# Kernel tuning notes

Hardware: AMD Instinct MI355X
Metric: run time of the kernel (lower is better)

## Reference

```python
import jax, jax.numpy as jnp
import numpy as np

N = 200000
D = 256
B = 512  # fixed num_segments (batch.max()+1 in the torch code)
LN_EPS = 1e-5


def _layernorm(h, gamma, beta):
    mu = jnp.mean(h, axis=-1, keepdims=True)
    var = jnp.var(h, axis=-1, keepdims=True)
    return (h - mu) * jax.lax.rsqrt(var + LN_EPS) * gamma + beta


def setup_inputs() -> dict:
    key = jax.random.key(0)
    ks = jax.random.split(key, 10)
    x = jax.random.normal(ks[0], (N, D), dtype=jnp.float32)
    batch = jnp.sort(jax.random.randint(ks[1], (N,), 0, B)).astype(jnp.int64)
    s = 0.05
    return {
        "x": x,
        "batch": batch,
        "vn_embed": jax.random.normal(ks[2], (1, D), dtype=jnp.float32) * 0.02,
        "W1": jax.random.normal(ks[3], (D, D), dtype=jnp.float32) * s,
        "b1": jnp.zeros((D,), dtype=jnp.float32),
        "g1": jnp.ones((D,), dtype=jnp.float32),
        "be1": jnp.zeros((D,), dtype=jnp.float32),
        "W2": jax.random.normal(ks[4], (D, D), dtype=jnp.float32) * s,
        "b2": jnp.zeros((D,), dtype=jnp.float32),
        "g2": jnp.ones((D,), dtype=jnp.float32),
        "be2": jnp.zeros((D,), dtype=jnp.float32),
        "Wg": jax.random.normal(ks[5], (2 * D, D), dtype=jnp.float32) * s,
        "bg": jnp.zeros((D,), dtype=jnp.float32),
    }


def reference(x, batch, vn_embed, W1, b1, g1, be1, W2, b2, g2, be2, Wg, bg):
    # scatter-mean: per-graph average of node features  [B, D]
    seg_sum = jax.ops.segment_sum(x, batch, num_segments=B)
    cnt = jax.ops.segment_sum(jnp.ones((x.shape[0],), x.dtype), batch, num_segments=B)
    node_agg = seg_sum / jnp.maximum(cnt, 1.0)[:, None]
    # node_to_vn: Linear + GELU(exact) + LayerNorm (dropout = identity at eval)
    vn_update = _layernorm(jax.nn.gelu(node_agg @ W1 + b1, approximate=False), g1, be1)
    vn_state = vn_embed + vn_update  # vn_embed broadcasts [1,D] -> [B,D]
    # gather broadcast back to nodes + vn_to_node MLP
    vn_broadcast = vn_state[batch]  # [N, D]
    node_update = _layernorm(jax.nn.gelu(vn_broadcast @ W2 + b2, approximate=False), g2, be2)
    # sigmoid gate on concat + gated residual
    gate = jax.nn.sigmoid(jnp.concatenate([x, node_update], axis=-1) @ Wg + bg)
    x_out = x + gate * node_update
    return (x_out, vn_state)
```

## Files before the change

### kernel.cpp

```cpp
#include <hip/hip_runtime.h>
#include <hip/hip_bf16.h>
#include <math.h>

#define DIM 256
#define B_SEG 512
#define LN_EPS 1e-5f
#define CHUNK 64

typedef __attribute__((ext_vector_type(8))) short bf16x8;
typedef __attribute__((ext_vector_type(4))) float f32x4;

__device__ __forceinline__ float gelu_exact(float v) {
    return 0.5f * v * (1.0f + erff(v * 0.70710678118654752f));
}

__device__ __forceinline__ unsigned int pack2bf(float a, float b) {
    unsigned int ua = (unsigned int)__bfloat16_as_ushort(__float2bfloat16(a));
    unsigned int ub = (unsigned int)__bfloat16_as_ushort(__float2bfloat16(b));
    return ua | (ub << 16);
}

__device__ __forceinline__ void async16(const void* g, void* l) {
    __builtin_amdgcn_global_load_lds(
        (const __attribute__((address_space(1))) void*)(g),
        (__attribute__((address_space(3))) void*)(l), 16, 0, 0);
}

__global__ __launch_bounds__(256) void k_wprep(const float* __restrict__ Wg,
                                               __hip_bfloat16* __restrict__ Wt2) {
    int k = blockIdx.x;
    int c = threadIdx.x;
    Wt2[((size_t)(k >> 3) << 11) + (c << 3) + (k & 7)] = __float2bfloat16(Wg[(size_t)k * DIM + c]);
}

__global__ __launch_bounds__(256) void k_segsum(const float* __restrict__ x,
                                                const int* __restrict__ batch,
                                                float* __restrict__ sums,
                                                float* __restrict__ cnt,
                                                __hip_bfloat16* __restrict__ xbf,
                                                int n, int emit) {
    const int i0 = blockIdx.x * CHUNK;
    if (i0 >= n) return;
    const int t    = threadIdx.x;
    const int lane = t & 63;
    const int d4   = lane * 4;
    const int rg   = t >> 6;

    int   bt[16];
    float4 v[16];
    #pragma unroll
    for (int j = 0; j < 16; ++j) {
        int i = i0 + rg + 4 * j;
        bt[j] = (i < n) ? batch[i] : -1;
    }
    #pragma unroll
    for (int j = 0; j < 16; ++j) {
        int i = i0 + rg + 4 * j;
        v[j] = (i < n) ? *(const float4*)(x + (size_t)i * DIM + d4)
                       : make_float4(0.f, 0.f, 0.f, 0.f);
    }

    if (emit) {
        #pragma unroll
        for (int j = 0; j < 16; ++j) {
            int i = i0 + rg + 4 * j;
            if (i < n) {
                uint2 pk;
                pk.x = pack2bf(v[j].x, v[j].y);
                pk.y = pack2bf(v[j].z, v[j].w);
                *(uint2*)((char*)xbf + (size_t)i * 512 + ((d4 * 2) ^ ((i & 7) << 4))) = pk;
            }
        }
    }

    float4 acc = make_float4(0.f, 0.f, 0.f, 0.f);
    int cur = -1, run = 0;
    #pragma unroll
    for (int j = 0; j < 16; ++j) {
        if (bt[j] != cur) {
            if (cur >= 0) {
                atomicAdd(&sums[(size_t)cur * DIM + d4 + 0], acc.x);
                atomicAdd(&sums[(size_t)cur * DIM + d4 + 1], acc.y);
                atomicAdd(&sums[(size_t)cur * DIM + d4 + 2], acc.z);
                atomicAdd(&sums[(size_t)cur * DIM + d4 + 3], acc.w);
                if (d4 == 0) atomicAdd(&cnt[cur], (float)run);
            }
            acc = make_float4(0.f, 0.f, 0.f, 0.f);
            run = 0; cur = bt[j];
        }
        acc.x += v[j].x; acc.y += v[j].y; acc.z += v[j].z; acc.w += v[j].w;
        run++;
    }
    if (cur >= 0) {
        atomicAdd(&sums[(size_t)cur * DIM + d4 + 0], acc.x);
        atomicAdd(&sums[(size_t)cur * DIM + d4 + 1], acc.y);
        atomicAdd(&sums[(size_t)cur * DIM + d4 + 2], acc.z);
        atomicAdd(&sums[(size_t)cur * DIM + d4 + 3], acc.w);
        if (d4 == 0) atomicAdd(&cnt[cur], (float)run);
    }
}

__global__ __launch_bounds__(256) void k_vn(const float* __restrict__ sums,
                                            const float* __restrict__ cnt,
                                            const float* __restrict__ vn_embed,
                                            const float* __restrict__ W1, const float* __restrict__ b1,
                                            const float* __restrict__ g1, const float* __restrict__ be1,
                                            const float* __restrict__ W2, const float* __restrict__ b2,
                                            const float* __restrict__ g2, const float* __restrict__ be2,
                                            const float* __restrict__ Wg, const float* __restrict__ bg,
                                            float* __restrict__ vn_state_out,
                                            float* __restrict__ nu,
                                            float* __restrict__ gpart) {
    __shared__ float sIn[DIM];
    __shared__ float sRed[DIM];
    __shared__ float sRed2[DIM];
    const int b = blockIdx.x;
    const int d = threadIdx.x;

    float c = cnt[b];
    float denom = fmaxf(c, 1.0f);
    sIn[d] = sums[(size_t)b * DIM + d] / denom;
    __syncthreads();

    float h0 = 0.f, h1 = 0.f, h2a = 0.f, h3 = 0.f;
    for (int k = 0; k < DIM; k += 4) {
        h0  = fmaf(sIn[k + 0], W1[(size_t)(k + 0) * DIM + d], h0);
        h1  = fmaf(sIn[k + 1], W1[(size_t)(k + 1) * DIM + d], h1);
        h2a = fmaf(sIn[k + 2], W1[(size_t)(k + 2) * DIM + d], h2a);
        h3  = fmaf(sIn[k + 3], W1[(size_t)(k + 3) * DIM + d], h3);
    }
    float h = gelu_exact(b1[d] + ((h0 + h1) + (h2a + h3)));

    sRed[d] = h; sRed2[d] = h * h;
    __syncthreads();
    for (int s = 128; s > 0; s >>= 1) {
        if (d < s) { sRed[d] += sRed[d + s]; sRed2[d] += sRed2[d + s]; }
        __syncthreads();
    }
    float mu = sRed[0] * (1.0f / DIM);
    float var = fmaxf(sRed2[0] * (1.0f / DIM) - mu * mu, 0.0f);
    float rs = rsqrtf(var + LN_EPS);
    float vnst = vn_embed[d] + ((h - mu) * rs * g1[d] + be1[d]);
    vn_state_out[(size_t)b * DIM + d] = vnst;
    __syncthreads();
    sIn[d] = vnst;
    __syncthreads();

    float g0 = 0.f, g1a = 0.f, g2a = 0.f, g3 = 0.f;
    for (int k = 0; k < DIM; k += 4) {
        g0  = fmaf(sIn[k + 0], W2[(size_t)(k + 0) * DIM + d], g0);
        g1a = fmaf(sIn[k + 1], W2[(size_t)(k + 1) * DIM + d], g1a);
        g2a = fmaf(sIn[k + 2], W2[(size_t)(k + 2) * DIM + d], g2a);
        g3  = fmaf(sIn[k + 3], W2[(size_t)(k + 3) * DIM + d], g3);
    }
    float h2 = gelu_exact(b2[d] + ((g0 + g1a) + (g2a + g3)));

    sRed[d] = h2; sRed2[d] = h2 * h2;
    __syncthreads();
    for (int s = 128; s > 0; s >>= 1) {
        if (d < s) { sRed[d] += sRed[d + s]; sRed2[d] += sRed2[d + s]; }
        __syncthreads();
    }
    float mu2 = sRed[0] * (1.0f / DIM);
    float var2 = fmaxf(sRed2[0] * (1.0f / DIM) - mu2 * mu2, 0.0f);
    float rs2 = rsqrtf(var2 + LN_EPS);
    float nud = (h2 - mu2) * rs2 * g2[d] + be2[d];
    nu[(size_t)b * DIM + d] = nud;
    __syncthreads();
    sIn[d] = nud;
    __syncthreads();

    float p0 = 0.f, p1 = 0.f, p2 = 0.f, p3 = 0.f;
    for (int k = 0; k < DIM; k += 4) {
        p0 = fmaf(sIn[k + 0], Wg[(size_t)(DIM + k + 0) * DIM + d], p0);
        p1 = fmaf(sIn[k + 1], Wg[(size_t)(DIM + k + 1) * DIM + d], p1);
        p2 = fmaf(sIn[k + 2], Wg[(size_t)(DIM + k + 2) * DIM + d], p2);
        p3 = fmaf(sIn[k + 3], Wg[(size_t)(DIM + k + 3) * DIM + d], p3);
    }
    gpart[(size_t)b * DIM + d] = bg[d] + ((p0 + p1) + (p2 + p3));
}

__global__ __launch_bounds__(256, 4) void k_gate_bf(const __hip_bfloat16* __restrict__ xbf,
                                                    const int* __restrict__ batch,
                                                    const __hip_bfloat16* __restrict__ Wt2,
                                                    const float* __restrict__ nu,
                                                    const float* __restrict__ gpart,
                                                    float* __restrict__ xout,
                                                    int n) {
    __shared__ __align__(16) char sA[64 * 512];

    const int tid  = threadIdx.x;
    const int wave = tid >> 6;
    const int lane = tid & 63;
    const int r15  = lane & 15;
    const int kq   = lane >> 4;
    const size_t i0 = (size_t)blockIdx.x * 64;

    const char* gsrc = (const char*)xbf + i0 * 512;
    #pragma unroll
    for (int j = 0; j < 8; ++j)
        async16(gsrc + j * 4096 + tid * 16, sA + j * 4096 + wave * 1024);
    __syncthreads();

    f32x4 acc[4][4];
    #pragma unroll
    for (int m = 0; m < 4; ++m)
        #pragma unroll
        for (int nn = 0; nn < 4; ++nn)
            acc[m][nn] = (f32x4){0.f, 0.f, 0.f, 0.f};

    #pragma unroll
    for (int ks = 0; ks < 8; ++ks) {
        bf16x8 a[4], b[4];
        #pragma unroll
        for (int nn = 0; nn < 4; ++nn) {
            int c = wave * 64 + nn * 16 + r15;
            b[nn] = *(const bf16x8*)(Wt2 + ((size_t)(ks * 4 + kq) << 11) + (c << 3));
        }
        #pragma unroll
        for (int m = 0; m < 4; ++m) {
            int r = m * 16 + r15;
            a[m] = *(const bf16x8*)(sA + r * 512 + ((ks * 64 + kq * 16) ^ ((r & 7) << 4)));
        }
        #pragma unroll
        for (int m = 0; m < 4; ++m)
            #pragma unroll
            for (int nn = 0; nn < 4; ++nn)
                acc[m][nn] = __builtin_amdgcn_mfma_f32_16x16x32_bf16(a[m], b[nn], acc[m][nn], 0, 0, 0);
    }

    #pragma unroll
    for (int m = 0; m < 4; ++m) {
        #pragma unroll
        for (int q = 0; q < 4; ++q) {
            int rr = m * 16 + kq * 4 + q;
            long node = (long)(i0 + rr);
            if (node >= n) continue;
            int bb = batch[node];
            #pragma unroll
            for (int nn = 0; nn < 4; ++nn) {
                int col = wave * 64 + nn * 16 + r15;
                float pre = acc[m][nn][q] + gpart[bb * DIM + col];
                float e = __expf(-pre);
                float gte = __builtin_amdgcn_rcpf(1.0f + e);
                float xres = __bfloat162float(
                    *(const __hip_bfloat16*)(sA + rr * 512 + ((2 * col) ^ ((rr & 7) << 4))));
                xout[(size_t)node * DIM + col] = xres + gte * nu[bb * DIM + col];
            }
        }
    }
}

__global__ __launch_bounds__(256) void k_gate_fp(const float* __restrict__ x,
                                                 const int* __restrict__ batch,
                                                 const __hip_bfloat16* __restrict__ Wt2,
                                                 const float* __restrict__ nu,
                                                 const float* __restrict__ gpart,
                                                 float* __restrict__ xout,
                                                 int n) {
    __shared__ __align__(16) char sA[32 * 512];

    const int tid  = threadIdx.x;
    const int wave = tid >> 6;
    const int lane = tid & 63;
    const int r15  = lane & 15;
    const int kq   = lane >> 4;
    const int i0   = blockIdx.x * 32;

    float4 av0[4], av1[4];
    #pragma unroll
    for (int j = 0; j < 4; ++j) {
        int v = j * 256 + tid;
        int r = v >> 5;
        int k8 = v & 31;
        int node = i0 + r;
        if (node < n) {
            const float* p = x + (size_t)node * DIM + k8 * 8;
            av0[j] = *(const float4*)p;
            av1[j] = *(const float4*)(p + 4);
        } else {
            av0[j] = make_float4(0.f, 0.f, 0.f, 0.f);
            av1[j] = av0[j];
        }
    }
    #pragma unroll
    for (int j = 0; j < 4; ++j) {
        int v = j * 256 + tid;
        int r = v >> 5;
        int k8 = v & 31;
        uint4 pk;
        pk.x = pack2bf(av0[j].x, av0[j].y);
        pk.y = pack2bf(av0[j].z, av0[j].w);
        pk.z = pack2bf(av1[j].x, av1[j].y);
        pk.w = pack2bf(av1[j].z, av1[j].w);
        *(uint4*)(sA + r * 512 + ((k8 * 16) ^ ((r & 7) << 4))) = pk;
    }
    __syncthreads();

    f32x4 acc[2][4];
    #pragma unroll
    for (int m = 0; m < 2; ++m)
        #pragma unroll
        for (int nn = 0; nn < 4; ++nn)
            acc[m][nn] = (f32x4){0.f, 0.f, 0.f, 0.f};

    #pragma unroll
    for (int ks = 0; ks < 8; ++ks) {
        bf16x8 a[2], b[4];
        #pragma unroll
        for (int nn = 0; nn < 4; ++nn) {
            int c = wave * 64 + nn * 16 + r15;
            b[nn] = *(const bf16x8*)(Wt2 + ((size_t)(ks * 4 + kq) << 11) + (c << 3));
        }
        #pragma unroll
        for (int m = 0; m < 2; ++m) {
            int r = m * 16 + r15;
            a[m] = *(const bf16x8*)(sA + r * 512 + ((ks * 64 + kq * 16) ^ ((r & 7) << 4)));
        }
        #pragma unroll
        for (int m = 0; m < 2; ++m)
            #pragma unroll
            for (int nn = 0; nn < 4; ++nn)
                acc[m][nn] = __builtin_amdgcn_mfma_f32_16x16x32_bf16(a[m], b[nn], acc[m][nn], 0, 0, 0);
    }

    #pragma unroll
    for (int m = 0; m < 2; ++m) {
        #pragma unroll
        for (int q = 0; q < 4; ++q) {
            int rr = m * 16 + kq * 4 + q;
            int node = i0 + rr;
            if (node >= n) continue;
            int bb = batch[node];
            #pragma unroll
            for (int nn = 0; nn < 4; ++nn) {
                int col = wave * 64 + nn * 16 + r15;
                float pre = acc[m][nn][q] + gpart[bb * DIM + col];
                float e = __expf(-pre);
                float gte = __builtin_amdgcn_rcpf(1.0f + e);
                float xres = __bfloat162float(
                    *(const __hip_bfloat16*)(sA + rr * 512 + ((2 * col) ^ ((rr & 7) << 4))));
                xout[(size_t)node * DIM + col] = xres + gte * nu[bb * DIM + col];
            }
        }
    }
}

extern "C" void kernel_launch(void* const* d_in, const int* in_sizes, int n_in,
                              void* d_out, int out_size, void* d_ws, size_t ws_size,
                              hipStream_t stream) {
    const float* x        = (const float*)d_in[0];
    const int*   batch    = (const int*)d_in[1];
    const float* vn_embed = (const float*)d_in[2];
    const float* W1  = (const float*)d_in[3];
    const float* b1  = (const float*)d_in[4];
    const float* g1  = (const float*)d_in[5];
    const float* be1 = (const float*)d_in[6];
    const float* W2  = (const float*)d_in[7];
    const float* b2  = (const float*)d_in[8];
    const float* g2  = (const float*)d_in[9];
    const float* be2 = (const float*)d_in[10];
    const float* Wg  = (const float*)d_in[11];
    const float* bg  = (const float*)d_in[12];

    const int n = in_sizes[0] / DIM;

    float* out = (float*)d_out;
    float* xout = out;
    float* vn_state_out = out + (size_t)n * DIM;

    float* ws    = (float*)d_ws;
    float* sums  = ws;
    float* cnt   = sums + (size_t)B_SEG * DIM;
    float* nu    = cnt + B_SEG;
    float* gpart = nu + (size_t)B_SEG * DIM;
    __hip_bfloat16* Wt2 = (__hip_bfloat16*)(gpart + (size_t)B_SEG * DIM);
    __hip_bfloat16* xbf = Wt2 + (size_t)DIM * DIM;

    const size_t base_bytes = ((size_t)B_SEG * DIM * 3 + B_SEG) * 4 + (size_t)DIM * DIM * 2;
    const int nt64 = (n + 63) / 64;
    const size_t need = base_bytes + (size_t)nt64 * 64 * 512;
    const bool use_bf = (ws_size >= need);

    hipMemsetAsync(d_ws, 0, ((size_t)B_SEG * DIM + B_SEG) * sizeof(float), stream);

    k_wprep<<<DIM, DIM, 0, stream>>>(Wg, Wt2);

    int nblk1 = (n + CHUNK - 1) / CHUNK;
    k_segsum<<<nblk1, 256, 0, stream>>>(x, batch, sums, cnt, xbf, n, use_bf ? 1 : 0);

    k_vn<<<B_SEG, 256, 0, stream>>>(sums, cnt, vn_embed,
                                    W1, b1, g1, be1,
                                    W2, b2, g2, be2,
                                    Wg, bg,
                                    vn_state_out, nu, gpart);

    if (use_bf) {
        k_gate_bf<<<nt64, 256, 0, stream>>>(xbf, batch, Wt2, nu, gpart, xout, n);
    } else {
        int nblk3 = (n + 31) / 32;
        k_gate_fp<<<nblk3, 256, 0, stream>>>(x, batch, Wt2, nu, gpart, xout, n);
    }
}
```

Measured before the change: 220.1 us.

## Split bf16 conversion from segment sum and sum from bf16 copy

Moves the fp32-to-bf16 conversion of x into its own grid-stride kernel. The segment-sum kernel then reads the bf16 copy with 16-byte loads instead of fp32. A separate fp32 segment-sum kernel covers the fallback path. The aim is to lighten the segsum kernel's registers and load width, at the cost of an extra kernel launch, an extra pass over the bf16 buffer, and segment means computed from bf16-rounded inputs.

```diff
diff --git a/kernel.cpp b/kernel.cpp
--- a/kernel.cpp
+++ b/kernel.cpp
@@ -5,7 +5,6 @@
 #define DIM 256
 #define B_SEG 512
 #define LN_EPS 1e-5f
-#define CHUNK 64
 
 typedef __attribute__((ext_vector_type(8))) short bf16x8;
 typedef __attribute__((ext_vector_type(4))) float f32x4;
@@ -18,6 +17,10 @@
     unsigned int ua = (unsigned int)__bfloat16_as_ushort(__float2bfloat16(a));
     unsigned int ub = (unsigned int)__bfloat16_as_ushort(__float2bfloat16(b));
     return ua | (ub << 16);
+}
+
+__device__ __forceinline__ float bf2f(short s) {
+    return __uint_as_float(((unsigned int)(unsigned short)s) << 16);
 }
 
 __device__ __forceinline__ void async16(const void* g, void* l) {
@@ -33,70 +36,94 @@
     Wt2[((size_t)(k >> 3) << 11) + (c << 3) + (k & 7)] = __float2bfloat16(Wg[(size_t)k * DIM + c]);
 }
 
-__global__ __launch_bounds__(256) void k_segsum(const float* __restrict__ x,
+__global__ __launch_bounds__(256) void k_convert(const float* __restrict__ x,
+                                                 __hip_bfloat16* __restrict__ xbf,
+                                                 int n) {
+    const int t    = threadIdx.x;
+    const int lane = t & 63;
+    const int rg   = t >> 6;
+    const int step = gridDim.x * 64;
+    for (int base = blockIdx.x * 64; base < n; base += step) {
+        const int r0 = base + rg * 16;
+        float4 v[16];
+        #pragma unroll
+        for (int j = 0; j < 16; ++j) {
+            int r = r0 + j;
+            v[j] = (r < n) ? *(const float4*)(x + (size_t)r * DIM + lane * 4)
+                           : make_float4(0.f, 0.f, 0.f, 0.f);
+        }
+        __builtin_amdgcn_sched_barrier(0);
+        #pragma unroll
+        for (int j = 0; j < 16; ++j) {
+            int r = r0 + j;
+            if (r < n) {
+                uint2 pk;
+                pk.x = pack2bf(v[j].x, v[j].y);
+                pk.y = pack2bf(v[j].z, v[j].w);
+                *(uint2*)((char*)xbf + (size_t)r * 512 + ((lane * 8) ^ ((r & 7) << 4))) = pk;
+            }
+        }
+    }
+}
+
+__global__ __launch_bounds__(256) void k_segsum(const __hip_bfloat16* __restrict__ xbf,
                                                 const int* __restrict__ batch,
                                                 float* __restrict__ sums,
                                                 float* __restrict__ cnt,
-                                                __hip_bfloat16* __restrict__ xbf,
-                                                int n, int emit) {
-    const int i0 = blockIdx.x * CHUNK;
+                                                int n) {
+    const int i0 = blockIdx.x * 64;
     if (i0 >= n) return;
     const int t    = threadIdx.x;
     const int lane = t & 63;
-    const int d4   = lane * 4;
     const int rg   = t >> 6;
-
-    int   bt[16];
-    float4 v[16];
-    #pragma unroll
-    for (int j = 0; j < 16; ++j) {
-        int i = i0 + rg + 4 * j;
-        bt[j] = (i < n) ? batch[i] : -1;
-    }
-    #pragma unroll
-    for (int j = 0; j < 16; ++j) {
-        int i = i0 + rg + 4 * j;
-        v[j] = (i < n) ? *(const float4*)(x + (size_t)i * DIM + d4)
-                       : make_float4(0.f, 0.f, 0.f, 0.f);
-    }
-
-    if (emit) {
-        #pragma unroll
-        for (int j = 0; j < 16; ++j) {
-            int i = i0 + rg + 4 * j;
-            if (i < n) {
-                uint2 pk;
-                pk.x = pack2bf(v[j].x, v[j].y);
-                pk.y = pack2bf(v[j].z, v[j].w);
-                *(uint2*)((char*)xbf + (size_t)i * 512 + ((d4 * 2) ^ ((i & 7) << 4))) = pk;
-            }
-        }
-    }
-
-    float4 acc = make_float4(0.f, 0.f, 0.f, 0.f);
+    const int half = lane >> 5;
+    const int li   = lane & 31;
+    const int d8   = li * 8;
+    const int R0   = i0 + rg * 16;
+
+    int    bt[8];
+    bf16x8 w[8];
+    #pragma unroll
+    for (int j = 0; j < 8; ++j) {
+        int r = R0 + half + 2 * j;
+        bt[j] = (r < n) ? batch[r] : -1;
+    }
+    #pragma unroll
+    for (int j = 0; j < 8; ++j) {
+        int r = R0 + half + 2 * j;
+        if (r < n) {
+            w[j] = *(const bf16x8*)((const char*)xbf + (size_t)r * 512 +
+                                    ((d8 * 2) ^ ((r & 7) << 4)));
+        } else {
+            w[j] = (bf16x8){0, 0, 0, 0, 0, 0, 0, 0};
+        }
+    }
+    __builtin_amdgcn_sched_barrier(0);
+
+    float acc[8] = {0.f, 0.f, 0.f, 0.f, 0.f, 0.f, 0.f, 0.f};
     int cur = -1, run = 0;
     #pragma unroll
-    for (int j = 0; j < 16; ++j) {
+    for (int j = 0; j < 8; ++j) {
         if (bt[j] != cur) {
             if (cur >= 0) {
-                atomicAdd(&sums[(size_t)cur * DIM + d4 + 0], acc.x);
-                atomicAdd(&sums[(size_t)cur * DIM + d4 + 1], acc.y);
-                atomicAdd(&sums[(size_t)cur * DIM + d4 + 2], acc.z);
-                atomicAdd(&sums[(size_t)cur * DIM + d4 + 3], acc.w);
-                if (d4 == 0) atomicAdd(&cnt[cur], (float)run);
+                #pragma unroll
+                for (int e = 0; e < 8; ++e)
+                    atomicAdd(&sums[(size_t)cur * DIM + d8 + e], acc[e]);
+                if (li == 0) atomicAdd(&cnt[cur], (float)run);
             }
-            acc = make_float4(0.f, 0.f, 0.f, 0.f);
+            #pragma unroll
+            for (int e = 0; e < 8; ++e) acc[e] = 0.f;
             run = 0; cur = bt[j];
         }
-        acc.x += v[j].x; acc.y += v[j].y; acc.z += v[j].z; acc.w += v[j].w;
+        #pragma unroll
+        for (int e = 0; e < 8; ++e) acc[e] += bf2f(w[j][e]);
         run++;
     }
     if (cur >= 0) {
-        atomicAdd(&sums[(size_t)cur * DIM + d4 + 0], acc.x);
-        atomicAdd(&sums[(size_t)cur * DIM + d4 + 1], acc.y);
-        atomicAdd(&sums[(size_t)cur * DIM + d4 + 2], acc.z);
-        atomicAdd(&sums[(size_t)cur * DIM + d4 + 3], acc.w);
-        if (d4 == 0) atomicAdd(&cnt[cur], (float)run);
+        #pragma unroll
+        for (int e = 0; e < 8; ++e)
+            atomicAdd(&sums[(size_t)cur * DIM + d8 + e], acc[e]);
+        if (li == 0) atomicAdd(&cnt[cur], (float)run);
     }
 }
 
@@ -251,6 +278,47 @@
     }
 }
 
+__global__ __launch_bounds__(256) void k_segsum_fp(const float* __restrict__ x,
+                                                   const int* __restrict__ batch,
+                                                   float* __restrict__ sums,
+                                                   float* __restrict__ cnt,
+                                                   int n) {
+    const int i0 = blockIdx.x * 64;
+    if (i0 >= n) return;
+    const int t    = threadIdx.x;
+    const int lane = t & 63;
+    const int d4   = lane * 4;
+    const int rg   = t >> 6;
+    float4 acc = make_float4(0.f, 0.f, 0.f, 0.f);
+    int cur = -1, run = 0;
+    for (int j = 0; j < 16; ++j) {
+        int i = i0 + rg + 4 * j;
+        if (i >= n) break;
+        int b = batch[i];
+        if (b != cur) {
+            if (cur >= 0) {
+                atomicAdd(&sums[(size_t)cur * DIM + d4 + 0], acc.x);
+                atomicAdd(&sums[(size_t)cur * DIM + d4 + 1], acc.y);
+                atomicAdd(&sums[(size_t)cur * DIM + d4 + 2], acc.z);
+                atomicAdd(&sums[(size_t)cur * DIM + d4 + 3], acc.w);
+                if (d4 == 0) atomicAdd(&cnt[cur], (float)run);
+            }
+            acc = make_float4(0.f, 0.f, 0.f, 0.f);
+            run = 0; cur = b;
+        }
+        float4 v = *(const float4*)(x + (size_t)i * DIM + d4);
+        acc.x += v.x; acc.y += v.y; acc.z += v.z; acc.w += v.w;
+        run++;
+    }
+    if (cur >= 0) {
+        atomicAdd(&sums[(size_t)cur * DIM + d4 + 0], acc.x);
+        atomicAdd(&sums[(size_t)cur * DIM + d4 + 1], acc.y);
+        atomicAdd(&sums[(size_t)cur * DIM + d4 + 2], acc.z);
+        atomicAdd(&sums[(size_t)cur * DIM + d4 + 3], acc.w);
+        if (d4 == 0) atomicAdd(&cnt[cur], (float)run);
+    }
+}
+
 __global__ __launch_bounds__(256) void k_gate_fp(const float* __restrict__ x,
                                                  const int* __restrict__ batch,
                                                  const __hip_bfloat16* __restrict__ Wt2,
@@ -259,7 +327,6 @@
                                                  float* __restrict__ xout,
                                                  int n) {
     __shared__ __align__(16) char sA[32 * 512];
-
     const int tid  = threadIdx.x;
     const int wave = tid >> 6;
     const int lane = tid & 63;
@@ -386,8 +453,13 @@
 
     k_wprep<<<DIM, DIM, 0, stream>>>(Wg, Wt2);
 
-    int nblk1 = (n + CHUNK - 1) / CHUNK;
-    k_segsum<<<nblk1, 256, 0, stream>>>(x, batch, sums, cnt, xbf, n, use_bf ? 1 : 0);
+    if (use_bf) {
+        int cblk = (nt64 < 2048) ? nt64 : 2048;
+        k_convert<<<cblk, 256, 0, stream>>>(x, xbf, n);
+        k_segsum<<<nt64, 256, 0, stream>>>(xbf, batch, sums, cnt, n);
+    } else {
+        k_segsum_fp<<<nt64, 256, 0, stream>>>(x, batch, sums, cnt, n);
+    }
 
     k_vn<<<B_SEG, 256, 0, stream>>>(sums, cnt, vn_embed,
                                     W1, b1, g1, be1,
```

Measured after the change: 404.9 us. 1.84x slower.
